# Kernel tuning notes

Hardware: AMD Instinct MI355X
Metric: run time of the kernel (lower is better)

The kernel has to match this reference:

```python
import jax, jax.numpy as jnp
import numpy as np

B, LQ, LKV = 4, 512, 8192
Q_DIM, KV_DIM = 1024, 512
QK_CH, V_CH, N_HEADS = 256, 256, 8
EPS = 1e-5


def _layernorm(x, g, b):
    m = jnp.mean(x, axis=-1, keepdims=True)
    v = jnp.mean(jnp.square(x - m), axis=-1, keepdims=True)
    return (x - m) * jax.lax.rsqrt(v + EPS) * g + b


def setup_inputs() -> dict:
    key = jax.random.key(0)
    ks = jax.random.split(key, 8)
    hidden_states = jax.random.normal(ks[0], (B, LQ, Q_DIM), dtype=jnp.float32)
    inputs = jax.random.normal(ks[1], (B, LKV, KV_DIM), dtype=jnp.float32)
    # Linear weights stored as [in, out] for x @ W
    Wq = jax.random.normal(ks[2], (Q_DIM, QK_CH), dtype=jnp.float32) * (1.0 / np.sqrt(Q_DIM))
    Wk = jax.random.normal(ks[3], (KV_DIM, QK_CH), dtype=jnp.float32) * (1.0 / np.sqrt(KV_DIM))
    Wv = jax.random.normal(ks[4], (KV_DIM, V_CH), dtype=jnp.float32) * (1.0 / np.sqrt(KV_DIM))
    bq = jnp.zeros((QK_CH,), jnp.float32)
    bk = jax.random.normal(ks[5], (QK_CH,), dtype=jnp.float32) * 0.02
    bv = jax.random.normal(ks[6], (V_CH,), dtype=jnp.float32) * 0.02
    ln1_g = jnp.ones((Q_DIM,), jnp.float32)
    ln1_b = jnp.zeros((Q_DIM,), jnp.float32)
    ln2_g = jnp.ones((KV_DIM,), jnp.float32)
    ln2_b = jnp.zeros((KV_DIM,), jnp.float32)
    return dict(hidden_states=hidden_states, inputs=inputs,
                ln1_g=ln1_g, ln1_b=ln1_b, ln2_g=ln2_g, ln2_b=ln2_b,
                Wq=Wq, bq=bq, Wk=Wk, bk=bk, Wv=Wv, bv=bv)


def reference(hidden_states, inputs, ln1_g, ln1_b, ln2_g, ln2_b,
              Wq, bq, Wk, bk, Wv, bv):
    H = N_HEADS
    dqk = QK_CH // H
    dv = V_CH // H
    hs = _layernorm(hidden_states, ln1_g, ln1_b)          # [B,LQ,Q_DIM]
    inp = _layernorm(inputs, ln2_g, ln2_b)                # [B,LKV,KV_DIM]
    q = (hs @ Wq + bq).reshape(B, LQ, H, dqk)             # [B,LQ,H,dqk]
    k = (inp @ Wk + bk).reshape(B, LKV, H, dqk)           # [B,LKV,H,dqk]
    v = (inp @ Wv + bv).reshape(B, LKV, H, dv)            # [B,LKV,H,dv]
    scores = jnp.einsum('bqhd,bkhd->bhqk', q, k) / np.sqrt(dqk).astype(np.float32)
    probs = jax.nn.softmax(scores, axis=-1)               # [B,H,LQ,LKV] (materialized, as in torch)
    ctx = jnp.einsum('bhqk,bkhd->bqhd', probs, v)         # [B,LQ,H,dv]
    return ctx.reshape(B, LQ, H * dv)
```

## Files before the change

kernel.cpp:

```cpp
#include <hip/hip_runtime.h>
#include <hip/hip_bf16.h>
#include <math.h>

#define NB    4
#define LQ    512
#define LKV   8192
#define QDIM  1024
#define KVDIM 512
#define NH    8
#define EPS_LN 1e-5f
#define SMAX  12.0f

typedef __attribute__((ext_vector_type(8))) short bf16x8;
typedef __attribute__((ext_vector_type(4))) float f32x4;

static __device__ __forceinline__ ushort f2bf(float x) {
    unsigned int u = __builtin_bit_cast(unsigned int, x);
    u += 0x7FFFu + ((u >> 16) & 1u);
    return (ushort)(u >> 16);
}

#if __has_builtin(__builtin_amdgcn_cvt_pk_bf16_f32)
static __device__ __forceinline__ unsigned int pk_bf16(float a, float b) {
    auto r = __builtin_amdgcn_cvt_pk_bf16_f32(a, b);
    return __builtin_bit_cast(unsigned int, r);
}
#else
static __device__ __forceinline__ unsigned int pk_bf16(float a, float b) {
    return (unsigned int)f2bf(a) | ((unsigned int)f2bf(b) << 16);
}
#endif

#if __has_builtin(__builtin_amdgcn_exp2f)
#define EXP2F(x) __builtin_amdgcn_exp2f(x)
#else
#define EXP2F(x) exp2f(x)
#endif

static __device__ __forceinline__ void interleave_swap(unsigned int &x, unsigned int &y, int lane) {
#if __has_builtin(__builtin_amdgcn_permlane32_swap) && __has_builtin(__builtin_amdgcn_permlane16_swap)
    {
        auto r1 = __builtin_amdgcn_permlane32_swap(x, y, false, false);
        auto r2 = __builtin_amdgcn_permlane16_swap(r1[0], r1[1], false, false);
        x = (unsigned int)r2[0];
        y = (unsigned int)r2[1];
    }
#else
    {
        unsigned int xs = (unsigned int)__shfl_xor((int)x, 32, 64);
        unsigned int ys = (unsigned int)__shfl_xor((int)y, 32, 64);
        unsigned int A2 = (lane & 32) ? ys : x;
        unsigned int C2 = (lane & 32) ? y  : xs;
        unsigned int A2x = (unsigned int)__shfl_xor((int)A2, 16, 64);
        unsigned int C2x = (unsigned int)__shfl_xor((int)C2, 16, 64);
        x = (lane & 16) ? C2x : A2;
        y = (lane & 16) ? C2  : A2x;
    }
#endif
}

static __device__ __forceinline__ void gld_lds16(const ushort* g, ushort* l) {
    __builtin_amdgcn_global_load_lds(
        (const __attribute__((address_space(1))) unsigned int*)g,
        (__attribute__((address_space(3))) unsigned int*)l, 16, 0, 0);
}

template<int K>
static __device__ __forceinline__ void ln_norm_row(
    const float* __restrict__ x, const float* __restrict__ g,
    const float* __restrict__ bta, ushort* __restrict__ y, int row, int lane)
{
    const float* xp = x + (size_t)row * K;
    constexpr int NV = K / 256;
    float4 v[NV];
    float s = 0.f;
#pragma unroll
    for (int i = 0; i < NV; ++i) {
        v[i] = *(const float4*)(xp + lane * 4 + i * 256);
        s += v[i].x + v[i].y + v[i].z + v[i].w;
    }
#pragma unroll
    for (int o = 1; o < 64; o <<= 1) s += __shfl_xor(s, o, 64);
    const float mu = s * (1.0f / K);
    float vs = 0.f;
#pragma unroll
    for (int i = 0; i < NV; ++i) {
        float dx = v[i].x - mu, dy = v[i].y - mu, dz = v[i].z - mu, dw = v[i].w - mu;
        vs += dx * dx + dy * dy + dz * dz + dw * dw;
    }
#pragma unroll
    for (int o = 1; o < 64; o <<= 1) vs += __shfl_xor(vs, o, 64);
    const float rs = rsqrtf(vs * (1.0f / K) + EPS_LN);
#pragma unroll
    for (int i = 0; i < NV; ++i) {
        const float4 gv = *(const float4*)(g   + lane * 4 + i * 256);
        const float4 bv = *(const float4*)(bta + lane * 4 + i * 256);
        uint2 o;
        o.x = pk_bf16((v[i].x - mu) * rs * gv.x + bv.x, (v[i].y - mu) * rs * gv.y + bv.y);
        o.y = pk_bf16((v[i].z - mu) * rs * gv.z + bv.z, (v[i].w - mu) * rs * gv.w + bv.w);
        *(uint2*)(y + (size_t)row * K + lane * 4 + i * 256) = o;
    }
}

static __device__ __forceinline__ void ln_stats_row(
    const float* __restrict__ x, float* __restrict__ mean, float* __restrict__ rstd,
    int row, int lane)
{
    const float* xp = x + (size_t)row * QDIM;
    float4 v[4];
    float s = 0.f;
#pragma unroll
    for (int i = 0; i < 4; ++i) {
        v[i] = *(const float4*)(xp + lane * 4 + i * 256);
        s += v[i].x + v[i].y + v[i].z + v[i].w;
    }
#pragma unroll
    for (int o = 1; o < 64; o <<= 1) s += __shfl_xor(s, o, 64);
    const float mu = s * (1.0f / QDIM);
    float vs = 0.f;
#pragma unroll
    for (int i = 0; i < 4; ++i) {
        float dx = v[i].x - mu, dy = v[i].y - mu, dz = v[i].z - mu, dw = v[i].w - mu;
        vs += dx * dx + dy * dy + dz * dz + dw * dw;
    }
#pragma unroll
    for (int o = 1; o < 64; o <<= 1) vs += __shfl_xor(vs, o, 64);
    if (lane == 0) {
        mean[row] = mu;
        rstd[row] = rsqrtf(vs * (1.0f / QDIM) + EPS_LN);
    }
}

static __device__ __forceinline__ void wt_transpose_body(
    const float* __restrict__ src, ushort* __restrict__ dst, int K,
    int kx, int ny, int t, ushort (*Ts)[72])
{
    const int k0 = kx * 64, n0 = ny * 64;
    const int nl = t & 63;
#pragma unroll
    for (int p = 0; p < 16; ++p) {
        const int kl = p * 4 + (t >> 6);
        Ts[nl][kl] = f2bf(src[(size_t)(k0 + kl) * 256 + n0 + nl]);
    }
    __syncthreads();
    const int ck = (t & 7) * 8;
#pragma unroll
    for (int p = 0; p < 2; ++p) {
        const int rn = p * 32 + (t >> 3);
        *(bf16x8*)(dst + (size_t)(n0 + rn) * K + k0 + ck) = *(const bf16x8*)&Ts[rn][ck];
    }
}

__global__ __launch_bounds__(256) void phaseA_kernel(
    const float* __restrict__ inputs, const float* __restrict__ ln2g,
    const float* __restrict__ ln2b,   ushort* __restrict__ Abf,
    const float* __restrict__ hidden, float* __restrict__ mean_h, float* __restrict__ rstd_h,
    const float* __restrict__ Wq, const float* __restrict__ Wk, const float* __restrict__ Wv,
    ushort* __restrict__ WtQ, ushort* __restrict__ WtKV)
{
    __shared__ ushort Ts[64][72];
    const int bid = blockIdx.x;
    const int t = threadIdx.x;
    const int lane = t & 63;
    if (bid < 8192) {
        ln_norm_row<KVDIM>(inputs, ln2g, ln2b, Abf, bid * 4 + (t >> 6), lane);
    } else if (bid < 8704) {
        ln_stats_row(hidden, mean_h, rstd_h, (bid - 8192) * 4 + (t >> 6), lane);
    } else if (bid < 8768) {
        const int p = bid - 8704;
        wt_transpose_body(Wq, WtQ, QDIM, p & 15, p >> 4, t, Ts);
    } else if (bid < 8800) {
        const int p = bid - 8768;
        wt_transpose_body(Wk, WtKV, KVDIM, p & 7, p >> 3, t, Ts);
    } else {
        const int p = bid - 8800;
        wt_transpose_body(Wv, WtKV + (size_t)256 * KVDIM, KVDIM, p & 7, p >> 3, t, Ts);
    }
}

__global__ __launch_bounds__(256) void phaseB_kernel(
    const ushort* __restrict__ Abf, const ushort* __restrict__ WtKV,
    const float* __restrict__ bk, const float* __restrict__ bv,
    ushort* __restrict__ kb, ushort* __restrict__ vt,
    const float* __restrict__ hidden, const float* __restrict__ mean_h,
    const float* __restrict__ rstd_h,
    const float* __restrict__ ln1g, const float* __restrict__ ln1b,
    const ushort* __restrict__ WtQ, const float* __restrict__ bq,
    ushort* __restrict__ qb, float oscale)
{
    __shared__ __align__(16) ushort SMEM[4 * 64 * 72];
    const int bid  = blockIdx.x;
    const int t    = threadIdx.x;
    const int lane = t & 63;
    const int w    = t >> 6;
    const int lq   = lane & 15;
    const int lg   = lane >> 4;
    const int wm   = w >> 1;
    const int wn   = w & 1;

    if (bid < 1024) {
        const int bm = (bid >> 2) * 128;
        const int bn = (bid & 3) * 128;
        ushort* As = SMEM;
        ushort* Bs = SMEM + 8192;

        const int srow = t >> 3;
        const int scol = ((t & 7) ^ (srow & 7)) * 8;
        const ushort* gA = Abf  + (size_t)(bm + srow) * KVDIM + scol;
        const ushort* gB = WtKV + (size_t)(bn + srow) * KVDIM + scol;

        f32x4 acc[4][4] = {};
        for (int k0 = 0; k0 < KVDIM; k0 += 64) {
#pragma unroll
            for (int p = 0; p < 4; ++p) {
                gld_lds16(gA + (size_t)(p * 32) * KVDIM + k0, As + p * 2048 + t * 8);
                gld_lds16(gB + (size_t)(p * 32) * KVDIM + k0, Bs + p * 2048 + t * 8);
            }
            __syncthreads();
#pragma unroll
            for (int kh = 0; kh < 2; ++kh) {
                bf16x8 af[4], bf[4];
#pragma unroll
                for (int mt = 0; mt < 4; ++mt) {
                    const int m = wm * 64 + mt * 16 + lq;
                    af[mt] = *(const bf16x8*)(As + m * 64 + (((lg + 4 * kh) ^ (m & 7)) << 3));
                }
#pragma unroll
                for (int nt = 0; nt < 4; ++nt) {
                    const int n = wn * 64 + nt * 16 + lq;
                    bf[nt] = *(const bf16x8*)(Bs + n * 64 + (((lg + 4 * kh) ^ (n & 7)) << 3));
                }
#pragma unroll
                for (int mt = 0; mt < 4; ++mt)
#pragma unroll
                    for (int nt = 0; nt < 4; ++nt)
                        acc[mt][nt] = __builtin_amdgcn_mfma_f32_16x16x32_bf16(af[mt], bf[nt], acc[mt][nt], 0, 0, 0);
            }
            __syncthreads();
        }
        const int m0base = bm + wm * 64;
        const int bidx   = m0base >> 13;
        const int tokb   = m0base & 8191;

        if (bn < 256) {
            ushort (*Cs)[72] = (ushort(*)[72])(SMEM + w * 64 * 72);
#pragma unroll
            for (int nt = 0; nt < 4; ++nt) {
                const int n_l = nt * 16 + lq;
                const float bias = bk[bn + wn * 64 + n_l];
#pragma unroll
                for (int mt = 0; mt < 4; ++mt)
#pragma unroll
                    for (int r = 0; r < 4; ++r)
                        Cs[mt * 16 + lg * 4 + r][n_l] = f2bf(acc[mt][nt][r] + bias);
            }
            const int r0 = lane >> 3;
            const int ck = (lane & 7) * 8;
            const int nc = bn + wn * 64 + ck;
            const int h = nc >> 5, d = nc & 31;
            const size_t obase = (((size_t)(bidx * NH + h) << 13) + tokb) * 32 + d;
#pragma unroll
            for (int p = 0; p < 8; ++p) {
                const int row = p * 8 + r0;
                *(bf16x8*)(kb + obase + (size_t)row * 32) = *(const bf16x8*)&Cs[row][ck];
            }
        } else {
            ushort (*Cs)[72] = (ushort(*)[72])(SMEM + w * 64 * 72);
#pragma unroll
            for (int nt = 0; nt < 4; ++nt) {
                const int n_l = nt * 16 + lq;
                const float bias = bv[(bn - 256) + wn * 64 + n_l];
#pragma unroll
                for (int mt = 0; mt < 4; ++mt) {
                    uint2 o;
                    o.x = pk_bf16(acc[mt][nt][0] + bias, acc[mt][nt][1] + bias);
                    o.y = pk_bf16(acc[mt][nt][2] + bias, acc[mt][nt][3] + bias);
                    *(uint2*)&Cs[n_l][mt * 16 + lg * 4] = o;
                }
            }
            const int r0 = lane >> 3;
            const int cm = (lane & 7) * 8;
            const int tokc = tokb + cm;
#pragma unroll
            for (int p = 0; p < 8; ++p) {
                const int row = p * 8 + r0;
                const int nv  = (bn - 256) + wn * 64 + row;
                const int h = nv >> 5, d = nv & 31;
                *(bf16x8*)(vt + ((size_t)(bidx * NH + h) * 32 + d) * LKV + tokc) =
                    *(const bf16x8*)&Cs[row][cm];
            }
        }
    } else {
        const int p  = bid - 1024;
        const int bm = (p >> 2) * 64;
        const int bn = (p & 3) * 64;
        ushort* As = SMEM;
        ushort* Bs = SMEM + 4096;

        const int srow = t >> 3;
        const int scol = ((t & 7) ^ (srow & 7)) * 8;
        const ushort* gB = WtQ + (size_t)(bn + srow) * QDIM + scol;
        ushort* lB  = Bs + t * 8;
        ushort* lA0 = As + t * 8;
        ushort* lA1 = As + 2048 + t * 8;

        const int r0 = bm + srow;
        const float mu0 = mean_h[r0],      rs0 = rstd_h[r0];
        const float mu1 = mean_h[r0 + 32], rs1 = rstd_h[r0 + 32];
        const float* xA0 = hidden + (size_t)r0 * QDIM + scol;
        const float* xA1 = xA0 + (size_t)32 * QDIM;

        f32x4 acc[2][2] = {};
        for (int k0 = 0; k0 < QDIM; k0 += 64) {
            gld_lds16(gB + k0,                      lB);
            gld_lds16(gB + (size_t)32 * QDIM + k0,  lB + 2048);
            const float4 a0 = *(const float4*)(xA0 + k0);
            const float4 a1 = *(const float4*)(xA0 + k0 + 4);
            const float4 c0 = *(const float4*)(xA1 + k0);
            const float4 c1 = *(const float4*)(xA1 + k0 + 4);
            const float4 g0 = *(const float4*)(ln1g + k0 + scol);
            const float4 g1 = *(const float4*)(ln1g + k0 + scol + 4);
            const float4 d0 = *(const float4*)(ln1b + k0 + scol);
            const float4 d1 = *(const float4*)(ln1b + k0 + scol + 4);
            uint4 w0, w1;
            w0.x = pk_bf16((a0.x - mu0) * rs0 * g0.x + d0.x, (a0.y - mu0) * rs0 * g0.y + d0.y);
            w0.y = pk_bf16((a0.z - mu0) * rs0 * g0.z + d0.z, (a0.w - mu0) * rs0 * g0.w + d0.w);
            w0.z = pk_bf16((a1.x - mu0) * rs0 * g1.x + d1.x, (a1.y - mu0) * rs0 * g1.y + d1.y);
            w0.w = pk_bf16((a1.z - mu0) * rs0 * g1.z + d1.z, (a1.w - mu0) * rs0 * g1.w + d1.w);
            w1.x = pk_bf16((c0.x - mu1) * rs1 * g0.x + d0.x, (c0.y - mu1) * rs1 * g0.y + d0.y);
            w1.y = pk_bf16((c0.z - mu1) * rs1 * g0.z + d0.z, (c0.w - mu1) * rs1 * g0.w + d0.w);
            w1.z = pk_bf16((c1.x - mu1) * rs1 * g1.x + d1.x, (c1.y - mu1) * rs1 * g1.y + d1.y);
            w1.w = pk_bf16((c1.z - mu1) * rs1 * g1.z + d1.z, (c1.w - mu1) * rs1 * g1.w + d1.w);
            *(uint4*)lA0 = w0;
            *(uint4*)lA1 = w1;
            __syncthreads();
#pragma unroll
            for (int kh = 0; kh < 2; ++kh) {
                bf16x8 af[2], bf[2];
#pragma unroll
                for (int mt = 0; mt < 2; ++mt) {
                    const int m = wm * 32 + mt * 16 + lq;
                    af[mt] = *(const bf16x8*)(As + m * 64 + (((lg + 4 * kh) ^ (m & 7)) << 3));
                }
#pragma unroll
                for (int nt = 0; nt < 2; ++nt) {
                    const int n = wn * 32 + nt * 16 + lq;
                    bf[nt] = *(const bf16x8*)(Bs + n * 64 + (((lg + 4 * kh) ^ (n & 7)) << 3));
                }
#pragma unroll
                for (int mt = 0; mt < 2; ++mt)
#pragma unroll
                    for (int nt = 0; nt < 2; ++nt)
                        acc[mt][nt] = __builtin_amdgcn_mfma_f32_16x16x32_bf16(af[mt], bf[nt], acc[mt][nt], 0, 0, 0);
            }
            __syncthreads();
        }

#pragma unroll
        for (int nt = 0; nt < 2; ++nt) {
            const int n = bn + wn * 32 + nt * 16 + lq;
            const int h = n >> 5, d = n & 31;
            const float bias = bq[n];
#pragma unroll
            for (int mt = 0; mt < 2; ++mt) {
                const int m0   = bm + wm * 32 + mt * 16 + lg * 4;
                const int bidx = m0 >> 9;
                const int tok  = m0 & 511;
                const size_t base = (((size_t)(bidx * NH + h) << 9) + tok) * 32 + d;
#pragma unroll
                for (int r = 0; r < 4; ++r)
                    qb[base + (size_t)r * 32] = f2bf((acc[mt][nt][r] + bias) * oscale);
            }
        }
    }
}

#define NQ 4
__global__ __launch_bounds__(256, 3) void attn_mfma_kernel(
    const ushort* __restrict__ Qb,
    const ushort* __restrict__ Kb,
    const ushort* __restrict__ Vt,
    float* __restrict__ Opart,
    float* __restrict__ lpart)
{
    const int bid = blockIdx.x;
    const int xcd = bid & 7;
    const int u   = bid >> 3;
    const int bhw = u >> 5;
    const int r2  = u & 31;
    const int qt  = r2 >> 2;
    const int quarter = r2 & 3;
    const int bh  = (bhw << 3) | xcd;
    const int t = threadIdx.x, w = t >> 6, lane = t & 63;
    const int lq = lane & 15, lg = lane >> 4;

    __shared__ __align__(16) float Ob[2 * 64 * 36];
    __shared__ float lbuf[4][64];

    bf16x8 qfrag[NQ];
    const size_t qbase = ((size_t)bh * LQ + qt * 64) * 32;
#pragma unroll
    for (int n = 0; n < NQ; ++n)
        qfrag[n] = *(const bf16x8*)(Qb + qbase + (size_t)(n * 16 + lq) * 32 + lg * 8);

    const int kv0 = quarter * 2048 + w * 512;
    const ushort* KpA = Kb + ((size_t)bh * LKV + kv0 + lq) * 32 + lg * 8;
    const ushort* VpA = Vt + ((size_t)bh * 32 + lq) * LKV + kv0 + lg * 8;

    f32x4 oacc[2][NQ] = {};
    float l_part[NQ] = {};
    const f32x4 cM = {-SMAX, -SMAX, -SMAX, -SMAX};

    for (int kt = 0; kt < 512; kt += 64) {
        bf16x8 kc[4];
#pragma unroll
        for (int m = 0; m < 4; ++m)
            kc[m] = *(const bf16x8*)(KpA + (size_t)(kt + m * 16) * 32);
        bf16x8 vc[2][2];
#pragma unroll
        for (int dt = 0; dt < 2; ++dt)
#pragma unroll
            for (int z = 0; z < 2; ++z)
                vc[dt][z] = *(const bf16x8*)(VpA + (size_t)(dt * 16) * LKV + kt + z * 32);

#pragma unroll
        for (int z = 0; z < 2; ++z) {
            f32x4 s2[2][NQ];
#pragma unroll
            for (int mm = 0; mm < 2; ++mm)
#pragma unroll
                for (int n = 0; n < NQ; ++n)
                    s2[mm][n] = __builtin_amdgcn_mfma_f32_16x16x32_bf16(kc[2 * z + mm], qfrag[n], cM, 0, 0, 0);

            bf16x8 pfz[NQ];
#pragma unroll
            for (int n = 0; n < NQ; ++n) {
                const float e0 = EXP2F(s2[0][n][0]);
                const float e1 = EXP2F(s2[0][n][1]);
                const float e2 = EXP2F(s2[0][n][2]);
                const float e3 = EXP2F(s2[0][n][3]);
                const float f0 = EXP2F(s2[1][n][0]);
                const float f1 = EXP2F(s2[1][n][1]);
                const float f2 = EXP2F(s2[1][n][2]);
                const float f3 = EXP2F(s2[1][n][3]);
                l_part[n] += ((e0 + e1) + (e2 + e3)) + ((f0 + f1) + (f2 + f3));
                unsigned int wa = pk_bf16(e0, e1);
                unsigned int wb = pk_bf16(e2, e3);
                unsigned int wc = pk_bf16(f0, f1);
                unsigned int wd = pk_bf16(f2, f3);
                interleave_swap(wa, wc, lane);
                interleave_swap(wb, wd, lane);
                uint4 wv;
                wv.x = wa; wv.y = wb; wv.z = wc; wv.w = wd;
                pfz[n] = __builtin_bit_cast(bf16x8, wv);
            }

#pragma unroll
            for (int dt = 0; dt < 2; ++dt)
#pragma unroll
                for (int n = 0; n < NQ; ++n)
                    oacc[dt][n] = __builtin_amdgcn_mfma_f32_16x16x32_bf16(vc[dt][z], pfz[n], oacc[dt][n], 0, 0, 0);
        }
    }

#pragma unroll
    for (int n = 0; n < NQ; ++n) {
        l_part[n] += __shfl_xor(l_part[n], 16);
        l_part[n] += __shfl_xor(l_part[n], 32);
    }
    if (lg == 0) {
#pragma unroll
        for (int n = 0; n < NQ; ++n)
            lbuf[w][n * 16 + lq] = l_part[n];
    }
    if (w >= 2) {
#pragma unroll
        for (int n = 0; n < NQ; ++n)
#pragma unroll
            for (int dt = 0; dt < 2; ++dt)
                *(f32x4*)&Ob[((size_t)(w - 2) * 64 + n * 16 + lq) * 36 + dt * 16 + lg * 4] = oacc[dt][n];
    }
    __syncthreads();
    if (w < 2) {
#pragma unroll
        for (int n = 0; n < NQ; ++n)
#pragma unroll
            for (int dt = 0; dt < 2; ++dt) {
                float* p = &Ob[((size_t)w * 64 + n * 16 + lq) * 36 + dt * 16 + lg * 4];
                f32x4 v = *(f32x4*)p;
                v += oacc[dt][n];
                *(f32x4*)p = v;
            }
    }
    __syncthreads();
    {
        const int pidx = (quarter * 32 + bh) * 8 + qt;
        const int q  = t >> 3;
        const int d0 = (t & 7) * 4;
#pragma unroll
        for (int rh = 0; rh < 2; ++rh) {
            const int row = q + rh * 32;
            f32x4 s0 = *(const f32x4*)&Ob[((size_t)row) * 36 + d0];
            f32x4 s1 = *(const f32x4*)&Ob[((size_t)(64 + row)) * 36 + d0];
            s0 += s1;
            *(f32x4*)(Opart + (size_t)pidx * 2048 + row * 32 + d0) = s0;
            if ((t & 7) == 0) {
                float gl = lbuf[0][row] + lbuf[1][row] + lbuf[2][row] + lbuf[3][row];
                lpart[(size_t)pidx * 64 + row] = gl;
            }
        }
    }
}

__global__ __launch_bounds__(256) void attn_combine_kernel(
    const float* __restrict__ Opart, const float* __restrict__ lpart,
    float* __restrict__ Out)
{
    const int cb = blockIdx.x;
    const int bh = cb >> 3, qt = cb & 7;
    const int b = bh >> 3, h = bh & 7;
    const int t = threadIdx.x;
    const int q = t >> 3;
    const int dq = (t & 7) * 4;
#pragma unroll
    for (int rh = 0; rh < 2; ++rh) {
        const int row = q + rh * 32;
        float4 o = {0.f, 0.f, 0.f, 0.f};
        float l = 0.f;
#pragma unroll
        for (int j = 0; j < 4; ++j) {
            const size_t pidx = (size_t)((j * 32 + bh) * 8 + qt);
            const float4 a = *(const float4*)(Opart + pidx * 2048 + row * 32 + dq);
            o.x += a.x; o.y += a.y; o.z += a.z; o.w += a.w;
            l += lpart[pidx * 64 + row];
        }
        const float inv = 1.0f / l;
        o.x *= inv; o.y *= inv; o.z *= inv; o.w *= inv;
        *(float4*)(Out + ((size_t)b * LQ + qt * 64 + row) * 256 + h * 32 + dq) = o;
    }
}

extern "C" void kernel_launch(void* const* d_in, const int* in_sizes, int n_in,
                              void* d_out, int out_size, void* d_ws, size_t ws_size,
                              hipStream_t stream)
{
    const float* hidden = (const float*)d_in[0];
    const float* inputs = (const float*)d_in[1];
    const float* ln1g   = (const float*)d_in[2];
    const float* ln1b   = (const float*)d_in[3];
    const float* ln2g   = (const float*)d_in[4];
    const float* ln2b   = (const float*)d_in[5];
    const float* Wq     = (const float*)d_in[6];
    const float* bq     = (const float*)d_in[7];
    const float* Wk     = (const float*)d_in[8];
    const float* bk     = (const float*)d_in[9];
    const float* Wv     = (const float*)d_in[10];
    const float* bv     = (const float*)d_in[11];
    float* out = (float*)d_out;

    char* wsb = (char*)d_ws;
    ushort* qb     = (ushort*)(wsb);
    ushort* WtKV   = (ushort*)(wsb + (1u << 20));
    ushort* WtQ    = (ushort*)(wsb + (1u << 20) + (512u << 10));
    float*  mean_h = (float*)(wsb + (2u << 20));
    float*  rstd_h = (float*)(wsb + (2u << 20) + 8192);
    ushort* kb     = (ushort*)(wsb + (2u << 20) + 16384);
    ushort* vt     = (ushort*)(wsb + (18u << 20) + 16384);
    ushort* Abf    = (ushort*)(wsb + (34u << 20) + 16384);

    float* Opart = (float*)Abf;
    float* lpart = Opart + (size_t)4 * 32 * 8 * 2048;

    const float oscale = 0.2550540226496112f;

    phaseA_kernel<<<8832, 256, 0, stream>>>(inputs, ln2g, ln2b, Abf,
                                            hidden, mean_h, rstd_h,
                                            Wq, Wk, Wv, WtQ, WtKV);
    phaseB_kernel<<<1152, 256, 0, stream>>>(Abf, WtKV, bk, bv, kb, vt,
                                            hidden, mean_h, rstd_h, ln1g, ln1b,
                                            WtQ, bq, qb, oscale);
    attn_mfma_kernel<<<1024, 256, 0, stream>>>(qb, kb, vt, Opart, lpart);
    attn_combine_kernel<<<256, 256, 0, stream>>>(Opart, lpart, out);
}
```

Before: 207.4 us.

## Shrink KV projection tiles to 64x128 with swizzled block order

Result: no change. 205.6 us (-0.8%).

```diff
diff --git a/kernel.cpp b/kernel.cpp
--- a/kernel.cpp
+++ b/kernel.cpp
@@ -178,7 +178,7 @@
     }
 }
 
-__global__ __launch_bounds__(256) void phaseB_kernel(
+__global__ __launch_bounds__(256, 3) void phaseB_kernel(
     const ushort* __restrict__ Abf, const ushort* __restrict__ WtKV,
     const float* __restrict__ bk, const float* __restrict__ bv,
     ushort* __restrict__ kb, ushort* __restrict__ vt,
@@ -198,100 +198,100 @@
     const int wm   = w >> 1;
     const int wn   = w & 1;
 
-    if (bid < 1024) {
-        const int bm = (bid >> 2) * 128;
-        const int bn = (bid & 3) * 128;
+    if (bid < 2048) {
+        const int work = ((bid & 7) << 8) | (bid >> 3);
+        const int bm = (work >> 2) * 64;
+        const int bn = (work & 3) * 128;
         ushort* As = SMEM;
-        ushort* Bs = SMEM + 8192;
+        ushort* Bs = SMEM + 4096;
 
         const int srow = t >> 3;
         const int scol = ((t & 7) ^ (srow & 7)) * 8;
         const ushort* gA = Abf  + (size_t)(bm + srow) * KVDIM + scol;
         const ushort* gB = WtKV + (size_t)(bn + srow) * KVDIM + scol;
 
-        f32x4 acc[4][4] = {};
+        f32x4 acc[4][2] = {};
         for (int k0 = 0; k0 < KVDIM; k0 += 64) {
-#pragma unroll
-            for (int p = 0; p < 4; ++p) {
-                gld_lds16(gA + (size_t)(p * 32) * KVDIM + k0, As + p * 2048 + t * 8);
+            gld_lds16(gA + k0,                      As + t * 8);
+            gld_lds16(gA + (size_t)32 * KVDIM + k0, As + 2048 + t * 8);
+#pragma unroll
+            for (int p = 0; p < 4; ++p)
                 gld_lds16(gB + (size_t)(p * 32) * KVDIM + k0, Bs + p * 2048 + t * 8);
-            }
             __syncthreads();
 #pragma unroll
             for (int kh = 0; kh < 2; ++kh) {
-                bf16x8 af[4], bf[4];
+                bf16x8 af[4], bf[2];
 #pragma unroll
                 for (int mt = 0; mt < 4; ++mt) {
-                    const int m = wm * 64 + mt * 16 + lq;
+                    const int m = mt * 16 + lq;
                     af[mt] = *(const bf16x8*)(As + m * 64 + (((lg + 4 * kh) ^ (m & 7)) << 3));
                 }
 #pragma unroll
-                for (int nt = 0; nt < 4; ++nt) {
-                    const int n = wn * 64 + nt * 16 + lq;
+                for (int nt = 0; nt < 2; ++nt) {
+                    const int n = w * 32 + nt * 16 + lq;
                     bf[nt] = *(const bf16x8*)(Bs + n * 64 + (((lg + 4 * kh) ^ (n & 7)) << 3));
                 }
 #pragma unroll
                 for (int mt = 0; mt < 4; ++mt)
 #pragma unroll
-                    for (int nt = 0; nt < 4; ++nt)
+                    for (int nt = 0; nt < 2; ++nt)
                         acc[mt][nt] = __builtin_amdgcn_mfma_f32_16x16x32_bf16(af[mt], bf[nt], acc[mt][nt], 0, 0, 0);
             }
             __syncthreads();
         }
-        const int m0base = bm + wm * 64;
-        const int bidx   = m0base >> 13;
-        const int tokb   = m0base & 8191;
+        const int bidx = bm >> 13;
+        const int tokb = bm & 8191;
+        const int nc0  = bn + w * 32;
 
         if (bn < 256) {
-            ushort (*Cs)[72] = (ushort(*)[72])(SMEM + w * 64 * 72);
-#pragma unroll
-            for (int nt = 0; nt < 4; ++nt) {
+            ushort* Cs = SMEM + w * 2560;
+#pragma unroll
+            for (int nt = 0; nt < 2; ++nt) {
                 const int n_l = nt * 16 + lq;
-                const float bias = bk[bn + wn * 64 + n_l];
+                const float bias = bk[nc0 + n_l];
 #pragma unroll
                 for (int mt = 0; mt < 4; ++mt)
 #pragma unroll
                     for (int r = 0; r < 4; ++r)
-                        Cs[mt * 16 + lg * 4 + r][n_l] = f2bf(acc[mt][nt][r] + bias);
-            }
-            const int r0 = lane >> 3;
-            const int ck = (lane & 7) * 8;
-            const int nc = bn + wn * 64 + ck;
-            const int h = nc >> 5, d = nc & 31;
-            const size_t obase = (((size_t)(bidx * NH + h) << 13) + tokb) * 32 + d;
-#pragma unroll
-            for (int p = 0; p < 8; ++p) {
-                const int row = p * 8 + r0;
-                *(bf16x8*)(kb + obase + (size_t)row * 32) = *(const bf16x8*)&Cs[row][ck];
+                        Cs[(mt * 16 + lg * 4 + r) * 40 + n_l] = f2bf(acc[mt][nt][r] + bias);
+            }
+            const int r0 = lane >> 2;
+            const int ck = (lane & 3) * 8;
+            const int h  = nc0 >> 5;
+            const size_t obase = (((size_t)(bidx * NH + h) << 13) + tokb) * 32 + ck;
+#pragma unroll
+            for (int p = 0; p < 4; ++p) {
+                const int row = p * 16 + r0;
+                *(bf16x8*)(kb + obase + (size_t)row * 32) = *(const bf16x8*)&Cs[row * 40 + ck];
             }
         } else {
-            ushort (*Cs)[72] = (ushort(*)[72])(SMEM + w * 64 * 72);
-#pragma unroll
-            for (int nt = 0; nt < 4; ++nt) {
+            ushort* Cs = SMEM + w * 2560;
+#pragma unroll
+            for (int nt = 0; nt < 2; ++nt) {
                 const int n_l = nt * 16 + lq;
-                const float bias = bv[(bn - 256) + wn * 64 + n_l];
+                const float bias = bv[(nc0 - 256) + n_l];
 #pragma unroll
                 for (int mt = 0; mt < 4; ++mt) {
                     uint2 o;
                     o.x = pk_bf16(acc[mt][nt][0] + bias, acc[mt][nt][1] + bias);
                     o.y = pk_bf16(acc[mt][nt][2] + bias, acc[mt][nt][3] + bias);
-                    *(uint2*)&Cs[n_l][mt * 16 + lg * 4] = o;
+                    *(uint2*)&Cs[n_l * 72 + mt * 16 + lg * 4] = o;
                 }
             }
             const int r0 = lane >> 3;
             const int cm = (lane & 7) * 8;
+            const int nv0 = nc0 - 256;
+            const int h  = nv0 >> 5;
             const int tokc = tokb + cm;
 #pragma unroll
-            for (int p = 0; p < 8; ++p) {
+            for (int p = 0; p < 4; ++p) {
                 const int row = p * 8 + r0;
-                const int nv  = (bn - 256) + wn * 64 + row;
-                const int h = nv >> 5, d = nv & 31;
-                *(bf16x8*)(vt + ((size_t)(bidx * NH + h) * 32 + d) * LKV + tokc) =
-                    *(const bf16x8*)&Cs[row][cm];
+                *(bf16x8*)(vt + ((size_t)(bidx * NH + h) * 32 + row) * LKV + tokc) =
+                    *(const bf16x8*)&Cs[row * 72 + cm];
             }
         }
     } else {
-        const int p  = bid - 1024;
+        const int p  = bid - 2048;
         const int bm = (p >> 2) * 64;
         const int bn = (p & 3) * 64;
         ushort* As = SMEM;
@@ -576,7 +576,7 @@
     phaseA_kernel<<<8832, 256, 0, stream>>>(inputs, ln2g, ln2b, Abf,
                                             hidden, mean_h, rstd_h,
                                             Wq, Wk, Wv, WtQ, WtKV);
-    phaseB_kernel<<<1152, 256, 0, stream>>>(Abf, WtKV, bk, bv, kb, vt,
+    phaseB_kernel<<<2176, 256, 0, stream>>>(Abf, WtKV, bk, bv, kb, vt,
                                             hidden, mean_h, rstd_h, ln1g, ln1b,
                                             WtQ, bq, qb, oscale);
     attn_mfma_kernel<<<1024, 256, 0, stream>>>(qb, kb, vt, Opart, lpart);
```
